# Kernel tuning notes

Measured on AMD Instinct MI355X. Metric: run time of the kernel, lower is better.

The kernel has to match this reference:

```python
import jax, jax.numpy as jnp
import numpy as np

# Production-scale sampled 2-hop GraphSAGE flow
N, C, HID, OUT = 1_000_000, 128, 32, 16
NSRC1, NDST1, E1 = 600_000, 80_000, 1_280_000
NDST2, E2 = 8_000, 80_000


def setup_inputs() -> dict:
    key = jax.random.key(0)
    ks = jax.random.split(key, 8)
    x = jax.random.normal(ks[0], (N, C), jnp.float32)
    n_id = jax.random.randint(ks[1], (NSRC1,), 0, N)
    src1 = jax.random.randint(ks[2], (E1,), 0, NSRC1)
    dst1 = jax.random.randint(ks[3], (E1,), 0, NDST1)
    src2 = jax.random.randint(ks[4], (E2,), 0, NDST1)
    dst2 = jax.random.randint(ks[5], (E2,), 0, NDST2)
    W1 = jax.random.normal(ks[6], (C, HID), jnp.float32) / np.sqrt(C).astype(np.float32)
    b1 = jnp.zeros((HID,), jnp.float32)
    W2 = jax.random.normal(ks[7], (HID, OUT), jnp.float32) / np.sqrt(HID).astype(np.float32)
    b2 = jnp.zeros((OUT,), jnp.float32)
    return dict(x=x, n_id=n_id, src1=src1, dst1=dst1, src2=src2, dst2=dst2,
                W1=W1, b1=b1, W2=W2, b2=b2)


def _mean_agg(feat_src, src, dst, num_dst):
    # scatter-mean of source features onto destination nodes (PyG aggr='mean')
    msg = feat_src[src]                                          # [E, F]
    s = jax.ops.segment_sum(msg, dst, num_segments=num_dst)      # [num_dst, F]
    cnt = jax.ops.segment_sum(jnp.ones((src.shape[0],), feat_src.dtype), dst,
                              num_segments=num_dst)
    return s / jnp.maximum(cnt, 1.0)[:, None]


def reference(x, n_id, src1, dst1, src2, dst2, W1, b1, W2, b2):
    h = x[n_id]                                  # gather sampled nodes [NSRC1, C]
    # SAGEConv(concat=False, normalize=False): mean-agg then linear
    h = _mean_agg(h, src1, dst1, NDST1) @ W1 + b1
    h = jax.nn.relu(h)                           # F.dropout(p=0.5) is a no-op in eval
    h = _mean_agg(h, src2, dst2, NDST2) @ W2 + b2
    return jax.nn.log_softmax(h, axis=1)
```

## Files before the change

### kernel.cpp

```cpp
#include <hip/hip_runtime.h>
#include <hip/hip_bf16.h>
#include <math.h>

#define N_NODES  1000000
#define C_IN     128
#define HID      32
#define OUTF     16
#define NSRC1    600000
#define NDST1    80000
#define E1       1280000
#define NDST2    8000
#define E2       80000

#define NB1 313

#define K1_STRIDE 36

__global__ __launch_bounds__(256) void k1_transform(
    const float* __restrict__ x, const int* __restrict__ n_id,
    const float* __restrict__ W1, float* __restrict__ p)
{
    __shared__ float W_s[C_IN * HID];
    __shared__ float A_t[4][32 * K1_STRIDE];

    for (int i = threadIdx.x; i < C_IN * HID; i += 256) W_s[i] = W1[i];
    __syncthreads();

    const int wave = threadIdx.x >> 6;
    const int lane = threadIdx.x & 63;
    const int gwave = blockIdx.x * 4 + wave;
    if (gwave >= NSRC1 / 32) return;
    const int s0 = gwave * 32;

    float* At = A_t[wave];

    int   mrow[4]; int f8[4]; const float* rowp[4];
    #pragma unroll
    for (int j = 0; j < 4; ++j) {
        int idx = j * 64 + lane;
        mrow[j] = idx >> 3;
        f8[j]   = idx & 7;
        rowp[j] = x + (size_t)n_id[s0 + mrow[j]] * C_IN + f8[j] * 4;
    }

    const int m4 = lane >> 3;
    const int o4 = lane & 7;

    float acc[4][4];
    #pragma unroll
    for (int i = 0; i < 4; ++i)
        #pragma unroll
        for (int j = 0; j < 4; ++j) acc[i][j] = 0.f;

    float4 v[4];
    #pragma unroll
    for (int j = 0; j < 4; ++j) v[j] = *(const float4*)(rowp[j]);

    #pragma unroll
    for (int c = 0; c < 4; ++c) {
        #pragma unroll
        for (int j = 0; j < 4; ++j) {
            int kb = f8[j] * 4;
            int m  = mrow[j];
            At[(kb + 0) * K1_STRIDE + m] = v[j].x;
            At[(kb + 1) * K1_STRIDE + m] = v[j].y;
            At[(kb + 2) * K1_STRIDE + m] = v[j].z;
            At[(kb + 3) * K1_STRIDE + m] = v[j].w;
        }
        if (c < 3) {
            #pragma unroll
            for (int j = 0; j < 4; ++j)
                v[j] = *(const float4*)(rowp[j] + (c + 1) * 32);
        }
        #pragma unroll 4
        for (int k = 0; k < 32; ++k) {
            float4 a = *(const float4*)&At[k * K1_STRIDE + m4 * 4];
            float4 w = *(const float4*)&W_s[(c * 32 + k) * HID + o4 * 4];
            acc[0][0] += a.x * w.x; acc[0][1] += a.x * w.y; acc[0][2] += a.x * w.z; acc[0][3] += a.x * w.w;
            acc[1][0] += a.y * w.x; acc[1][1] += a.y * w.y; acc[1][2] += a.y * w.z; acc[1][3] += a.y * w.w;
            acc[2][0] += a.z * w.x; acc[2][1] += a.z * w.y; acc[2][2] += a.z * w.z; acc[2][3] += a.z * w.w;
            acc[3][0] += a.w * w.x; acc[3][1] += a.w * w.y; acc[3][2] += a.w * w.z; acc[3][3] += a.w * w.w;
        }
    }

    #pragma unroll
    for (int i = 0; i < 4; ++i) {
        float4 o = make_float4(acc[i][0], acc[i][1], acc[i][2], acc[i][3]);
        *(float4*)&p[(size_t)(s0 + m4 * 4 + i) * HID + o4 * 4] = o;
    }
}

__global__ __launch_bounds__(256) void k_hist(
    const int* __restrict__ dst1, int* __restrict__ deg)
{
    const int e = blockIdx.x * 256 + threadIdx.x;
    if (e < E1) atomicAdd(&deg[dst1[e]], 1);
}

__global__ __launch_bounds__(256) void k_scan1(
    const int* __restrict__ deg, int* __restrict__ row_start,
    int* __restrict__ bsums)
{
    __shared__ int s[256];
    const int i = blockIdx.x * 256 + threadIdx.x;
    const int v = (i < NDST1) ? deg[i] : 0;
    s[threadIdx.x] = v;
    __syncthreads();
    #pragma unroll
    for (int off = 1; off < 256; off <<= 1) {
        int t = (threadIdx.x >= off) ? s[threadIdx.x - off] : 0;
        __syncthreads();
        s[threadIdx.x] += t;
        __syncthreads();
    }
    if (i < NDST1) row_start[i] = s[threadIdx.x] - v;
    if (threadIdx.x == 255) bsums[blockIdx.x] = s[255];
}

__global__ __launch_bounds__(512) void k_scan2(int* __restrict__ bsums)
{
    __shared__ int s[512];
    const int v = (threadIdx.x < NB1) ? bsums[threadIdx.x] : 0;
    s[threadIdx.x] = v;
    __syncthreads();
    #pragma unroll
    for (int off = 1; off < 512; off <<= 1) {
        int t = (threadIdx.x >= off) ? s[threadIdx.x - off] : 0;
        __syncthreads();
        s[threadIdx.x] += t;
        __syncthreads();
    }
    if (threadIdx.x < NB1) bsums[threadIdx.x] = s[threadIdx.x] - v;
}

__global__ __launch_bounds__(256) void k_apply(
    int* __restrict__ row_start, const int* __restrict__ bsums,
    int* __restrict__ cursor)
{
    const int i = blockIdx.x * 256 + threadIdx.x;
    if (i < NDST1) {
        int r = row_start[i] + bsums[blockIdx.x];
        row_start[i] = r;
        cursor[i] = r;
    }
}

__global__ __launch_bounds__(256) void k_bucket(
    const int* __restrict__ src1, const int* __restrict__ dst1,
    int* __restrict__ cursor, int* __restrict__ sorted_src)
{
    const int e = blockIdx.x * 256 + threadIdx.x;
    if (e >= E1) return;
    const int d = dst1[e];
    const int pos = atomicAdd(&cursor[d], 1);
    sorted_src[pos] = src1[e];
}

__global__ __launch_bounds__(256) void k_gather1(
    const int* __restrict__ row_start, const int* __restrict__ deg,
    const int* __restrict__ sorted_src, const float* __restrict__ p,
    const float* __restrict__ b1, const float* __restrict__ W2,
    float* __restrict__ q)
{
    __shared__ float w2s[HID * OUTF];
    __shared__ float b1s[HID];
    __shared__ float hbuf[8][HID];
    for (int i = threadIdx.x; i < HID * OUTF; i += 256) w2s[i] = W2[i];
    if (threadIdx.x < HID) b1s[threadIdx.x] = b1[threadIdx.x];
    __syncthreads();

    const int g = threadIdx.x >> 5;
    const int f = threadIdx.x & 31;
    const int d = blockIdx.x * 8 + g;
    if (d >= NDST1) return;

    const int start = row_start[d];
    const int dg    = deg[d];

    float acc = 0.f;
    int i = 0;
    for (; i + 2 <= dg; i += 2) {
        int s0 = sorted_src[start + i];
        int s1 = sorted_src[start + i + 1];
        acc += p[(size_t)s0 * HID + f] + p[(size_t)s1 * HID + f];
    }
    if (i < dg) acc += p[(size_t)sorted_src[start + i] * HID + f];

    const float h = fmaxf(acc / (float)max(dg, 1) + b1s[f], 0.f);
    hbuf[g][f] = h;
    if (f < OUTF) {
        float oacc = 0.f;
        #pragma unroll
        for (int k = 0; k < HID; ++k) oacc += hbuf[g][k] * w2s[k * OUTF + f];
        q[(size_t)d * OUTF + f] = oacc;
    }
}

__global__ __launch_bounds__(256) void k4_scatter2(
    const int* __restrict__ src2, const int* __restrict__ dst2,
    const float* __restrict__ q, float* __restrict__ agg2,
    float* __restrict__ cnt2)
{
    const int gid = blockIdx.x * 256 + threadIdx.x;
    const int e = gid >> 4;
    const int f = gid & 15;
    if (e >= E2) return;
    const int s = src2[e];
    const int d = dst2[e];
    atomicAdd(&agg2[(size_t)d * OUTF + f], q[(size_t)s * OUTF + f]);
    if (f == 0) atomicAdd(&cnt2[d], 1.0f);
}

__global__ __launch_bounds__(256) void k5_logsoftmax(
    const float* __restrict__ agg2, const float* __restrict__ cnt2,
    const float* __restrict__ b2, float* __restrict__ out)
{
    const int v = blockIdx.x * 256 + threadIdx.x;
    if (v >= NDST2) return;
    const float inv = 1.0f / fmaxf(cnt2[v], 1.0f);
    float z[OUTF];
    float m = -INFINITY;
    #pragma unroll
    for (int j = 0; j < OUTF; ++j) {
        z[j] = agg2[(size_t)v * OUTF + j] * inv + b2[j];
        m = fmaxf(m, z[j]);
    }
    float s = 0.f;
    #pragma unroll
    for (int j = 0; j < OUTF; ++j) s += expf(z[j] - m);
    const float lse = m + logf(s);
    #pragma unroll
    for (int j = 0; j < OUTF; ++j) out[(size_t)v * OUTF + j] = z[j] - lse;
}

extern "C" void kernel_launch(void* const* d_in, const int* in_sizes, int n_in,
                              void* d_out, int out_size, void* d_ws, size_t ws_size,
                              hipStream_t stream)
{
    const float* x    = (const float*)d_in[0];
    const int*   n_id = (const int*)  d_in[1];
    const int*   src1 = (const int*)  d_in[2];
    const int*   dst1 = (const int*)  d_in[3];
    const int*   src2 = (const int*)  d_in[4];
    const int*   dst2 = (const int*)  d_in[5];
    const float* W1   = (const float*)d_in[6];
    const float* b1   = (const float*)d_in[7];
    const float* W2   = (const float*)d_in[8];
    const float* b2   = (const float*)d_in[9];
    float* out = (float*)d_out;

    char* ws = (char*)d_ws;
    float* p          = (float*)(ws + 0);
    int*   sorted_src = (int*)  (ws + 76800000);
    int*   deg        = (int*)  (ws + 81920000);
    float* agg2       = (float*)(ws + 82240000);
    float* cnt2       = (float*)(ws + 82752000);
    int*   row_start  = (int*)  (ws + 82784000);
    int*   cursor     = (int*)  (ws + 83104032);
    int*   bsums      = (int*)  (ws + 83424032);
    float* q          = (float*)(ws + 83426080);

    hipMemsetAsync(deg, 0, 864000, stream);

    k1_transform <<<(NSRC1 / 32 + 3) / 4, 256, 0, stream>>>(x, n_id, W1, p);

    k_hist   <<<(E1 + 255) / 256, 256, 0, stream>>>(dst1, deg);
    k_scan1  <<<NB1, 256, 0, stream>>>(deg, row_start, bsums);
    k_scan2  <<<1, 512, 0, stream>>>(bsums);
    k_apply  <<<NB1, 256, 0, stream>>>(row_start, bsums, cursor);
    k_bucket <<<(E1 + 255) / 256, 256, 0, stream>>>(src1, dst1, cursor, sorted_src);

    k_gather1<<<(NDST1 + 7) / 8, 256, 0, stream>>>(row_start, deg, sorted_src,
                                                   p, b1, W2, q);

    k4_scatter2  <<<(E2 * 16 + 255) / 256, 256, 0, stream>>>(src2, dst2, q, agg2, cnt2);
    k5_logsoftmax<<<(NDST2 + 255) / 256, 256, 0, stream>>>(agg2, cnt2, b2, out);
}
```

Measured before the change: 853.9 us.

## Fuse transform with histograms, fp16 intermediate, atomic-offset scan, CSR second hop

```diff
diff --git a/kernel.cpp b/kernel.cpp
--- a/kernel.cpp
+++ b/kernel.cpp
@@ -1,5 +1,5 @@
 #include <hip/hip_runtime.h>
-#include <hip/hip_bf16.h>
+#include <hip/hip_fp16.h>
 #include <math.h>
 
 #define N_NODES  1000000
@@ -12,23 +12,49 @@
 #define NDST2    8000
 #define E2       80000
 
-#define NB1 313
+#define KB1 4688
+#define HB1 5000
+#define HB2 313
+#define AB1 313
+#define AB2 32
 
 #define K1_STRIDE 36
 
-__global__ __launch_bounds__(256) void k1_transform(
+__global__ __launch_bounds__(256) void kA_transform_hist(
     const float* __restrict__ x, const int* __restrict__ n_id,
-    const float* __restrict__ W1, float* __restrict__ p)
+    const float* __restrict__ W1, __half* __restrict__ p,
+    const int* __restrict__ dst1, const int* __restrict__ dst2,
+    int* __restrict__ deg1, int* __restrict__ deg2)
 {
     __shared__ float W_s[C_IN * HID];
     __shared__ float A_t[4][32 * K1_STRIDE];
 
+    const int bid = blockIdx.x;
+    int role, idx;
+    if (bid < 2 * KB1) { role = bid & 1; idx = bid >> 1; }
+    else {
+        int r = bid - 2 * KB1;
+        if (r < HB1 - KB1) { role = 1; idx = KB1 + r; }
+        else               { role = 2; idx = r - (HB1 - KB1); }
+    }
+
+    if (role == 1) {
+        int e = idx * 256 + threadIdx.x;
+        if (e < E1) atomicAdd(&deg1[dst1[e]], 1);
+        return;
+    }
+    if (role == 2) {
+        int e = idx * 256 + threadIdx.x;
+        if (e < E2) atomicAdd(&deg2[dst2[e]], 1);
+        return;
+    }
+
     for (int i = threadIdx.x; i < C_IN * HID; i += 256) W_s[i] = W1[i];
     __syncthreads();
 
     const int wave = threadIdx.x >> 6;
     const int lane = threadIdx.x & 63;
-    const int gwave = blockIdx.x * 4 + wave;
+    const int gwave = idx * 4 + wave;
     if (gwave >= NSRC1 / 32) return;
     const int s0 = gwave * 32;
 
@@ -37,9 +63,9 @@
     int   mrow[4]; int f8[4]; const float* rowp[4];
     #pragma unroll
     for (int j = 0; j < 4; ++j) {
-        int idx = j * 64 + lane;
-        mrow[j] = idx >> 3;
-        f8[j]   = idx & 7;
+        int i2 = j * 64 + lane;
+        mrow[j] = i2 >> 3;
+        f8[j]   = i2 & 7;
         rowp[j] = x + (size_t)n_id[s0 + mrow[j]] * C_IN + f8[j] * 4;
     }
 
@@ -85,152 +111,144 @@
 
     #pragma unroll
     for (int i = 0; i < 4; ++i) {
-        float4 o = make_float4(acc[i][0], acc[i][1], acc[i][2], acc[i][3]);
-        *(float4*)&p[(size_t)(s0 + m4 * 4 + i) * HID + o4 * 4] = o;
-    }
-}
-
-__global__ __launch_bounds__(256) void k_hist(
-    const int* __restrict__ dst1, int* __restrict__ deg)
-{
-    const int e = blockIdx.x * 256 + threadIdx.x;
-    if (e < E1) atomicAdd(&deg[dst1[e]], 1);
-}
-
-__global__ __launch_bounds__(256) void k_scan1(
-    const int* __restrict__ deg, int* __restrict__ row_start,
-    int* __restrict__ bsums)
-{
-    __shared__ int s[256];
-    const int i = blockIdx.x * 256 + threadIdx.x;
-    const int v = (i < NDST1) ? deg[i] : 0;
-    s[threadIdx.x] = v;
-    __syncthreads();
-    #pragma unroll
-    for (int off = 1; off < 256; off <<= 1) {
-        int t = (threadIdx.x >= off) ? s[threadIdx.x - off] : 0;
-        __syncthreads();
-        s[threadIdx.x] += t;
-        __syncthreads();
-    }
-    if (i < NDST1) row_start[i] = s[threadIdx.x] - v;
-    if (threadIdx.x == 255) bsums[blockIdx.x] = s[255];
-}
-
-__global__ __launch_bounds__(512) void k_scan2(int* __restrict__ bsums)
-{
-    __shared__ int s[512];
-    const int v = (threadIdx.x < NB1) ? bsums[threadIdx.x] : 0;
-    s[threadIdx.x] = v;
-    __syncthreads();
-    #pragma unroll
-    for (int off = 1; off < 512; off <<= 1) {
-        int t = (threadIdx.x >= off) ? s[threadIdx.x - off] : 0;
-        __syncthreads();
-        s[threadIdx.x] += t;
-        __syncthreads();
-    }
-    if (threadIdx.x < NB1) bsums[threadIdx.x] = s[threadIdx.x] - v;
-}
-
-__global__ __launch_bounds__(256) void k_apply(
-    int* __restrict__ row_start, const int* __restrict__ bsums,
-    int* __restrict__ cursor)
-{
-    const int i = blockIdx.x * 256 + threadIdx.x;
-    if (i < NDST1) {
-        int r = row_start[i] + bsums[blockIdx.x];
-        row_start[i] = r;
-        cursor[i] = r;
-    }
-}
-
-__global__ __launch_bounds__(256) void k_bucket(
+        union { __half2 h2[2]; uint2 u; } pk;
+        pk.h2[0] = __floats2half2_rn(acc[i][0], acc[i][1]);
+        pk.h2[1] = __floats2half2_rn(acc[i][2], acc[i][3]);
+        *(uint2*)&p[(size_t)(s0 + m4 * 4 + i) * HID + o4 * 4] = pk.u;
+    }
+}
+
+__global__ __launch_bounds__(256) void kB_alloc(
+    const int* __restrict__ deg1, const int* __restrict__ deg2,
+    int* __restrict__ rs1, int* __restrict__ rs2,
+    int* __restrict__ cur1, int* __restrict__ cur2,
+    int* __restrict__ counters)
+{
+    const int bid  = blockIdx.x;
+    const int lane = threadIdx.x & 63;
+    const int* deg; int* rs; int* cur; int* ctr; int nd; int d;
+    if (bid < AB1) { deg = deg1; rs = rs1; cur = cur1; ctr = counters + 0;
+                     nd = NDST1; d = bid * 256 + threadIdx.x; }
+    else           { deg = deg2; rs = rs2; cur = cur2; ctr = counters + 1;
+                     nd = NDST2; d = (bid - AB1) * 256 + threadIdx.x; }
+
+    int v = (d < nd) ? deg[d] : 0;
+    int incl = v;
+    #pragma unroll
+    for (int off = 1; off < 64; off <<= 1) {
+        int t = __shfl_up(incl, off, 64);
+        if (lane >= off) incl += t;
+    }
+    int total = __shfl(incl, 63, 64);
+    int base = 0;
+    if (lane == 63) base = atomicAdd(ctr, total);
+    base = __shfl(base, 63, 64);
+    if (d < nd) { int r = base + incl - v; rs[d] = r; cur[d] = r; }
+}
+
+__global__ __launch_bounds__(256) void kC_bucket(
     const int* __restrict__ src1, const int* __restrict__ dst1,
-    int* __restrict__ cursor, int* __restrict__ sorted_src)
-{
-    const int e = blockIdx.x * 256 + threadIdx.x;
-    if (e >= E1) return;
-    const int d = dst1[e];
-    const int pos = atomicAdd(&cursor[d], 1);
-    sorted_src[pos] = src1[e];
-}
-
-__global__ __launch_bounds__(256) void k_gather1(
+    const int* __restrict__ src2, const int* __restrict__ dst2,
+    int* __restrict__ cur1, int* __restrict__ cur2,
+    int* __restrict__ ss1, int* __restrict__ ss2)
+{
+    const int bid = blockIdx.x;
+    if (bid < HB1) {
+        int e = bid * 256 + threadIdx.x;
+        if (e < E1) {
+            int d = dst1[e];
+            int pos = atomicAdd(&cur1[d], 1);
+            ss1[pos] = src1[e];
+        }
+    } else {
+        int e = (bid - HB1) * 256 + threadIdx.x;
+        if (e < E2) {
+            int d = dst2[e];
+            int pos = atomicAdd(&cur2[d], 1);
+            ss2[pos] = src2[e];
+        }
+    }
+}
+
+__global__ __launch_bounds__(256) void kD_gather1(
     const int* __restrict__ row_start, const int* __restrict__ deg,
-    const int* __restrict__ sorted_src, const float* __restrict__ p,
+    const int* __restrict__ ss1, const __half* __restrict__ p,
     const float* __restrict__ b1, const float* __restrict__ W2,
     float* __restrict__ q)
 {
-    __shared__ float w2s[HID * OUTF];
-    __shared__ float b1s[HID];
-    __shared__ float hbuf[8][HID];
-    for (int i = threadIdx.x; i < HID * OUTF; i += 256) w2s[i] = W2[i];
-    if (threadIdx.x < HID) b1s[threadIdx.x] = b1[threadIdx.x];
-    __syncthreads();
-
-    const int g = threadIdx.x >> 5;
-    const int f = threadIdx.x & 31;
-    const int d = blockIdx.x * 8 + g;
-    if (d >= NDST1) return;
+    __shared__ float hbuf[16][HID + 1];
+    const int g = threadIdx.x >> 4;
+    const int f = threadIdx.x & 15;
+    const int d = blockIdx.x * 16 + g;
+
+    float w2r[HID];
+    #pragma unroll
+    for (int k = 0; k < HID; ++k) w2r[k] = W2[k * OUTF + f];
+    const float2 b1v = *(const float2*)&b1[2 * f];
 
     const int start = row_start[d];
     const int dg    = deg[d];
+    const __half2* ph2 = (const __half2*)p;
+
+    float2 acc = make_float2(0.f, 0.f);
+    int i = 0;
+    for (; i + 4 <= dg; i += 4) {
+        int s0 = ss1[start + i];
+        int s1 = ss1[start + i + 1];
+        int s2 = ss1[start + i + 2];
+        int s3 = ss1[start + i + 3];
+        float2 a = __half22float2(ph2[(size_t)s0 * 16 + f]);
+        float2 b = __half22float2(ph2[(size_t)s1 * 16 + f]);
+        float2 c = __half22float2(ph2[(size_t)s2 * 16 + f]);
+        float2 e = __half22float2(ph2[(size_t)s3 * 16 + f]);
+        acc.x += (a.x + b.x) + (c.x + e.x);
+        acc.y += (a.y + b.y) + (c.y + e.y);
+    }
+    for (; i < dg; ++i) {
+        float2 a = __half22float2(ph2[(size_t)ss1[start + i] * 16 + f]);
+        acc.x += a.x; acc.y += a.y;
+    }
+
+    const float inv = 1.f / (float)max(dg, 1);
+    hbuf[g][2 * f]     = fmaxf(acc.x * inv + b1v.x, 0.f);
+    hbuf[g][2 * f + 1] = fmaxf(acc.y * inv + b1v.y, 0.f);
+    float o = 0.f;
+    #pragma unroll
+    for (int k = 0; k < HID; ++k) o += hbuf[g][k] * w2r[k];
+    q[(size_t)d * OUTF + f] = o;
+}
+
+__global__ __launch_bounds__(256) void kE_gather2_lsm(
+    const int* __restrict__ row_start2, const int* __restrict__ deg2,
+    const int* __restrict__ ss2, const float* __restrict__ q,
+    const float* __restrict__ b2, float* __restrict__ out)
+{
+    const int g = threadIdx.x >> 4;
+    const int f = threadIdx.x & 15;
+    const int d = blockIdx.x * 16 + g;
+    if (d >= NDST2) return;
+
+    const int start = row_start2[d];
+    const int dg    = deg2[d];
 
     float acc = 0.f;
     int i = 0;
     for (; i + 2 <= dg; i += 2) {
-        int s0 = sorted_src[start + i];
-        int s1 = sorted_src[start + i + 1];
-        acc += p[(size_t)s0 * HID + f] + p[(size_t)s1 * HID + f];
-    }
-    if (i < dg) acc += p[(size_t)sorted_src[start + i] * HID + f];
-
-    const float h = fmaxf(acc / (float)max(dg, 1) + b1s[f], 0.f);
-    hbuf[g][f] = h;
-    if (f < OUTF) {
-        float oacc = 0.f;
-        #pragma unroll
-        for (int k = 0; k < HID; ++k) oacc += hbuf[g][k] * w2s[k * OUTF + f];
-        q[(size_t)d * OUTF + f] = oacc;
-    }
-}
-
-__global__ __launch_bounds__(256) void k4_scatter2(
-    const int* __restrict__ src2, const int* __restrict__ dst2,
-    const float* __restrict__ q, float* __restrict__ agg2,
-    float* __restrict__ cnt2)
-{
-    const int gid = blockIdx.x * 256 + threadIdx.x;
-    const int e = gid >> 4;
-    const int f = gid & 15;
-    if (e >= E2) return;
-    const int s = src2[e];
-    const int d = dst2[e];
-    atomicAdd(&agg2[(size_t)d * OUTF + f], q[(size_t)s * OUTF + f]);
-    if (f == 0) atomicAdd(&cnt2[d], 1.0f);
-}
-
-__global__ __launch_bounds__(256) void k5_logsoftmax(
-    const float* __restrict__ agg2, const float* __restrict__ cnt2,
-    const float* __restrict__ b2, float* __restrict__ out)
-{
-    const int v = blockIdx.x * 256 + threadIdx.x;
-    if (v >= NDST2) return;
-    const float inv = 1.0f / fmaxf(cnt2[v], 1.0f);
-    float z[OUTF];
-    float m = -INFINITY;
-    #pragma unroll
-    for (int j = 0; j < OUTF; ++j) {
-        z[j] = agg2[(size_t)v * OUTF + j] * inv + b2[j];
-        m = fmaxf(m, z[j]);
-    }
-    float s = 0.f;
-    #pragma unroll
-    for (int j = 0; j < OUTF; ++j) s += expf(z[j] - m);
-    const float lse = m + logf(s);
-    #pragma unroll
-    for (int j = 0; j < OUTF; ++j) out[(size_t)v * OUTF + j] = z[j] - lse;
+        int s0 = ss2[start + i];
+        int s1 = ss2[start + i + 1];
+        acc += q[(size_t)s0 * OUTF + f] + q[(size_t)s1 * OUTF + f];
+    }
+    if (i < dg) acc += q[(size_t)ss2[start + i] * OUTF + f];
+
+    float z = acc / (float)max(dg, 1) + b2[f];
+    float m = z;
+    #pragma unroll
+    for (int off = 8; off; off >>= 1) m = fmaxf(m, __shfl_xor(m, off, 16));
+    float e = expf(z - m);
+    float s = e;
+    #pragma unroll
+    for (int off = 8; off; off >>= 1) s += __shfl_xor(s, off, 16);
+    out[(size_t)d * OUTF + f] = z - m - logf(s);
 }
 
 extern "C" void kernel_launch(void* const* d_in, const int* in_sizes, int n_in,
@@ -250,29 +268,30 @@
     float* out = (float*)d_out;
 
     char* ws = (char*)d_ws;
-    float* p          = (float*)(ws + 0);
-    int*   sorted_src = (int*)  (ws + 76800000);
-    int*   deg        = (int*)  (ws + 81920000);
-    float* agg2       = (float*)(ws + 82240000);
-    float* cnt2       = (float*)(ws + 82752000);
-    int*   row_start  = (int*)  (ws + 82784000);
-    int*   cursor     = (int*)  (ws + 83104032);
-    int*   bsums      = (int*)  (ws + 83424032);
-    float* q          = (float*)(ws + 83426080);
-
-    hipMemsetAsync(deg, 0, 864000, stream);
-
-    k1_transform <<<(NSRC1 / 32 + 3) / 4, 256, 0, stream>>>(x, n_id, W1, p);
-
-    k_hist   <<<(E1 + 255) / 256, 256, 0, stream>>>(dst1, deg);
-    k_scan1  <<<NB1, 256, 0, stream>>>(deg, row_start, bsums);
-    k_scan2  <<<1, 512, 0, stream>>>(bsums);
-    k_apply  <<<NB1, 256, 0, stream>>>(row_start, bsums, cursor);
-    k_bucket <<<(E1 + 255) / 256, 256, 0, stream>>>(src1, dst1, cursor, sorted_src);
-
-    k_gather1<<<(NDST1 + 7) / 8, 256, 0, stream>>>(row_start, deg, sorted_src,
-                                                   p, b1, W2, q);
-
-    k4_scatter2  <<<(E2 * 16 + 255) / 256, 256, 0, stream>>>(src2, dst2, q, agg2, cnt2);
-    k5_logsoftmax<<<(NDST2 + 255) / 256, 256, 0, stream>>>(agg2, cnt2, b2, out);
-}
+    __half* p       = (__half*)(ws + 0);
+    int*   ss1      = (int*)   (ws + 38400000);
+    int*   ss2      = (int*)   (ws + 43520000);
+    int*   deg1     = (int*)   (ws + 43840000);
+    int*   deg2     = (int*)   (ws + 44160000);
+    int*   counters = (int*)   (ws + 44192000);
+    int*   rs1      = (int*)   (ws + 44192064);
+    int*   rs2      = (int*)   (ws + 44512064);
+    int*   cur1     = (int*)   (ws + 44544064);
+    int*   cur2     = (int*)   (ws + 44864064);
+    float* q        = (float*) (ws + 44896064);
+
+    hipMemsetAsync(deg1, 0, 352064, stream);
+
+    kA_transform_hist<<<2 * KB1 + (HB1 - KB1) + HB2, 256, 0, stream>>>(
+        x, n_id, W1, p, dst1, dst2, deg1, deg2);
+
+    kB_alloc <<<AB1 + AB2, 256, 0, stream>>>(deg1, deg2, rs1, rs2, cur1, cur2,
+                                             counters);
+
+    kC_bucket<<<HB1 + HB2, 256, 0, stream>>>(src1, dst1, src2, dst2,
+                                             cur1, cur2, ss1, ss2);
+
+    kD_gather1<<<NDST1 / 16, 256, 0, stream>>>(rs1, deg1, ss1, p, b1, W2, q);
+
+    kE_gather2_lsm<<<NDST2 / 16, 256, 0, stream>>>(rs2, deg2, ss2, q, b2, out);
+}
```

New measurement: 808.8 us. 5.3% less time.
